# Performance work log

Hardware: AMD Instinct MI355X
Metric: run time of the kernel (lower is better)

Reference implementation:

```python
import jax, jax.numpy as jnp
import numpy as np

B, N, D = 256, 50, 128
N_NODE, MAX_ATTR = 50000, 2000
ALPHA = 0.2  # LeakyReLU negative slope
STDV = 1.0 / np.sqrt(D)  # reset_parameters uniform(-stdv, stdv)
NEG = -9e15


def setup_inputs() -> dict:
    key = jax.random.key(0)
    ks = jax.random.split(key, 10)
    uni = lambda k, shp: jax.random.uniform(k, shp, jnp.float32, -STDV, STDV)
    return {
        "inputs": jax.random.randint(ks[0], (B, N), 0, N_NODE),
        "adj": jax.random.randint(ks[1], (B, N, N), 0, 5),
        "mask_item": jax.random.randint(ks[2], (B, N), 0, 2),
        "A_attr_sess": jax.random.normal(ks[3], (B, MAX_ATTR), jnp.float32),
        "embedding": uni(ks[4], (N_NODE, D)),
        "attr_embedding": uni(ks[5], (MAX_ATTR, D)),
        "a0": uni(ks[6], (D,)),
        "a1": uni(ks[7], (D,)),
        "a2": uni(ks[8], (D,)),
        "a3": uni(ks[9], (D,)),
    }


def reference(inputs, adj, mask_item, A_attr_sess, embedding, attr_embedding, a0, a1, a2, a3):
    h = embedding[inputs]  # [B, N, D]
    # (h.repeat(1,1,N) * h.repeat(1,N,1)).view(B,N,N,D) == outer elementwise product h_i * h_j
    a_in = jax.nn.leaky_relu(h[:, :, None, :] * h[:, None, :, :], ALPHA)  # [B,N,N,D]
    a_all = jnp.stack([a0, a1, a2, a3], axis=-1)  # [D, 4]
    e = jnp.einsum('bijd,dk->bijk', a_in, a_all)  # [B,N,N,4]
    alpha = jnp.full(adj.shape, NEG, dtype=e.dtype)
    alpha = jnp.where(adj == 1, e[..., 0], alpha)
    alpha = jnp.where(adj == 2, e[..., 1], alpha)
    alpha = jnp.where(adj == 3, e[..., 2], alpha)
    alpha = jnp.where(adj == 4, e[..., 3], alpha)
    alpha = jax.nn.softmax(alpha, axis=-1)
    output = jnp.einsum('bij,bjd->bid', alpha, h)  # [B, N, D]
    attr_sess = A_attr_sess @ attr_embedding  # [B, D]
    return output, attr_sess
```

## Files before the change

### kernel.cpp

```cpp
#include <hip/hip_runtime.h>
#include <math.h>

#define BB 256
#define NN 50
#define DD 128
#define MAXA 2000
#define NEGV -9e15f
#define NATTR 256

#define H_S   136
#define HT_S  72
#define AL_S  72

#define H_OFF   0
#define HT_OFF  (64 * H_S)
#define AL_OFF  (HT_OFF + 128 * HT_S)
#define ADJ_OFF (AL_OFF + 64 * AL_S)
#define LDS_US  (ADJ_OFF + 64 * 64)

typedef __attribute__((ext_vector_type(8))) short        s8b;
typedef __attribute__((ext_vector_type(4))) float        f32x4;
typedef __attribute__((ext_vector_type(4))) unsigned int u32x4;

static __device__ __forceinline__ unsigned short f2bf(float x) {
    unsigned int u = __float_as_uint(x);
    u = u + 0x7fffu + ((u >> 16) & 1u);
    return (unsigned short)(u >> 16);
}
static __device__ __forceinline__ float bf2f(unsigned int s) {
    return __uint_as_float(s << 16);
}
static __device__ __forceinline__ unsigned int pack2(float lo, float hi) {
    return (unsigned)f2bf(lo) | ((unsigned)f2bf(hi) << 16);
}
static __device__ __forceinline__ f32x4 mfma16(u32x4 a, u32x4 b, f32x4 c) {
    return __builtin_amdgcn_mfma_f32_16x16x32_bf16(
        __builtin_bit_cast(s8b, a), __builtin_bit_cast(s8b, b), c, 0, 0, 0);
}

__global__ __launch_bounds__(256) void sg_fused_kernel(
    const int* __restrict__ inputs,
    const int* __restrict__ adj,
    const float* __restrict__ A_attr,
    const float* __restrict__ embedding,
    const float* __restrict__ attr_emb,
    const float* __restrict__ a0,
    const float* __restrict__ a1,
    const float* __restrict__ a2,
    const float* __restrict__ a3,
    float* __restrict__ out,
    float* __restrict__ ws)
{
    __shared__ __align__(16) unsigned short sh[LDS_US];
    const int blk  = blockIdx.x;
    const int tid  = threadIdx.x;
    const int w    = tid >> 6;
    const int lane = tid & 63;
    const int g    = lane >> 4;
    const int c    = lane & 15;
    const int goff = g * 8;

    if (blk >= NATTR) {
        const int b = blk - NATTR;

        const int  i_   = lane;
        const bool live = (i_ < NN);
        int node = 0;
        if (live) node = inputs[b * NN + i_];
        float4 gv[8];
        #pragma unroll
        for (int n = 0; n < 8; ++n) {
            gv[n] = make_float4(0.f, 0.f, 0.f, 0.f);
            if (live) gv[n] = *(const float4*)(embedding + (size_t)node * DD + (w * 8 + n) * 4);
        }
        for (int idx = tid; idx < 4096; idx += 256) {
            const int i = idx >> 6, j = idx & 63;
            int a = 0;
            if (i < NN && j < NN) a = adj[(size_t)b * (NN * NN) + i * NN + j];
            sh[ADJ_OFF + idx] = (unsigned short)a;
        }
        #pragma unroll
        for (int n = 0; n < 8; ++n) {
            const int d4 = w * 8 + n;
            const unsigned short b0 = f2bf(gv[n].x), b1 = f2bf(gv[n].y);
            const unsigned short b2 = f2bf(gv[n].z), b3 = f2bf(gv[n].w);
            *(uint2*)(sh + H_OFF + i_ * H_S + d4 * 4) =
                make_uint2((unsigned)b0 | ((unsigned)b1 << 16),
                           (unsigned)b2 | ((unsigned)b3 << 16));
            sh[HT_OFF + (d4 * 4 + 0) * HT_S + i_] = b0;
            sh[HT_OFF + (d4 * 4 + 1) * HT_S + i_] = b1;
            sh[HT_OFF + (d4 * 4 + 2) * HT_S + i_] = b2;
            sh[HT_OFF + (d4 * 4 + 3) * HT_S + i_] = b3;
        }
        __syncthreads();

        u32x4 hA[4];
        float hf[4][8], hb[4][8];
        #pragma unroll
        for (int dt = 0; dt < 4; ++dt) {
            hA[dt] = *(const u32x4*)(const void*)(sh + H_OFF + (w * 16 + c) * H_S + dt * 32 + goff);
            #pragma unroll
            for (int p = 0; p < 4; ++p) {
                const unsigned int hp = hA[dt][p];
                hf[dt][2 * p]     = bf2f(hp & 0xffffu);
                hf[dt][2 * p + 1] = bf2f(hp >> 16);
                hb[dt][2 * p]     = fabsf(hf[dt][2 * p]);
                hb[dt][2 * p + 1] = fabsf(hf[dt][2 * p + 1]);
            }
        }
        f32x4 accS[4][4];
        #pragma unroll
        for (int jt = 0; jt < 4; ++jt)
            #pragma unroll
            for (int k = 0; k < 4; ++k) accS[jt][k] = (f32x4){0.f, 0.f, 0.f, 0.f};

        #pragma unroll
        for (int pass = 0; pass < 2; ++pass) {
            u32x4 Uf[4][2], Vf[4][2];
            #pragma unroll
            for (int kk = 0; kk < 2; ++kk) {
                const int k = pass * 2 + kk;
                const float* ap = (k == 0) ? a0 : (k == 1) ? a1 : (k == 2) ? a2 : a3;
                #pragma unroll
                for (int dt = 0; dt < 4; ++dt) {
                    const float4 aL = *(const float4*)(ap + dt * 32 + goff);
                    const float4 aH = *(const float4*)(ap + dt * 32 + goff + 4);
                    const float a8[8] = {aL.x, aL.y, aL.z, aL.w, aH.x, aH.y, aH.z, aH.w};
                    u32x4 U, V;
                    #pragma unroll
                    for (int p = 0; p < 4; ++p) {
                        U[p] = pack2(0.6f * a8[2 * p] * hf[dt][2 * p],
                                     0.6f * a8[2 * p + 1] * hf[dt][2 * p + 1]);
                        V[p] = pack2(0.4f * a8[2 * p] * hb[dt][2 * p],
                                     0.4f * a8[2 * p + 1] * hb[dt][2 * p + 1]);
                    }
                    Uf[dt][kk] = U; Vf[dt][kk] = V;
                }
            }
            #pragma unroll
            for (int jt = 0; jt < 4; ++jt) {
                #pragma unroll
                for (int dt = 0; dt < 4; ++dt) {
                    const u32x4 hB = *(const u32x4*)(const void*)(sh + H_OFF + (jt * 16 + c) * H_S + dt * 32 + goff);
                    u32x4 hBa;
                    #pragma unroll
                    for (int p = 0; p < 4; ++p) hBa[p] = hB[p] & 0x7fff7fffu;
                    accS[jt][pass * 2 + 0] = mfma16(Uf[dt][0], hB,  accS[jt][pass * 2 + 0]);
                    accS[jt][pass * 2 + 0] = mfma16(Vf[dt][0], hBa, accS[jt][pass * 2 + 0]);
                    accS[jt][pass * 2 + 1] = mfma16(Uf[dt][1], hB,  accS[jt][pass * 2 + 1]);
                    accS[jt][pass * 2 + 1] = mfma16(Vf[dt][1], hBa, accS[jt][pass * 2 + 1]);
                }
            }
        }

        float s_[4][4];
        #pragma unroll
        for (int jt = 0; jt < 4; ++jt) {
            #pragma unroll
            for (int reg = 0; reg < 4; ++reg) {
                const int il = w * 16 + g * 4 + reg;
                const int j  = jt * 16 + c;
                const int a  = (int)sh[ADJ_OFF + il * 64 + j];
                float sv = (a == 1) ? accS[jt][0][reg] : (a == 2) ? accS[jt][1][reg]
                         : (a == 3) ? accS[jt][2][reg] : (a == 4) ? accS[jt][3][reg] : NEGV;
                if (j >= NN) sv = -INFINITY;
                s_[jt][reg] = sv;
            }
        }
        #pragma unroll
        for (int reg = 0; reg < 4; ++reg) {
            float m = fmaxf(fmaxf(s_[0][reg], s_[1][reg]), fmaxf(s_[2][reg], s_[3][reg]));
            m = fmaxf(m, __shfl_xor(m, 1));
            m = fmaxf(m, __shfl_xor(m, 2));
            m = fmaxf(m, __shfl_xor(m, 4));
            m = fmaxf(m, __shfl_xor(m, 8));
            const float p0 = __expf(s_[0][reg] - m);
            const float p1 = __expf(s_[1][reg] - m);
            const float p2 = __expf(s_[2][reg] - m);
            const float p3 = __expf(s_[3][reg] - m);
            float sum = (p0 + p1) + (p2 + p3);
            sum += __shfl_xor(sum, 1);
            sum += __shfl_xor(sum, 2);
            sum += __shfl_xor(sum, 4);
            sum += __shfl_xor(sum, 8);
            const float r  = 1.0f / sum;
            const int  il  = w * 16 + g * 4 + reg;
            sh[AL_OFF + il * AL_S +  0 + c] = f2bf(p0 * r);
            sh[AL_OFF + il * AL_S + 16 + c] = f2bf(p1 * r);
            sh[AL_OFF + il * AL_S + 32 + c] = f2bf(p2 * r);
            sh[AL_OFF + il * AL_S + 48 + c] = f2bf(p3 * r);
        }

        const int il = w * 16 + c;
        const u32x4 pa0 = *(const u32x4*)(const void*)(sh + AL_OFF + il * AL_S + goff);
        const u32x4 pa1 = *(const u32x4*)(const void*)(sh + AL_OFF + il * AL_S + 32 + goff);
        #pragma unroll
        for (int nt = 0; nt < 8; ++nt) {
            const u32x4 v0 = *(const u32x4*)(const void*)(sh + HT_OFF + (nt * 16 + c) * HT_S + goff);
            const u32x4 v1 = *(const u32x4*)(const void*)(sh + HT_OFF + (nt * 16 + c) * HT_S + 32 + goff);
            f32x4 accp = (f32x4){0.f, 0.f, 0.f, 0.f};
            accp = mfma16(pa0, v0, accp);
            accp = mfma16(pa1, v1, accp);
            #pragma unroll
            for (int reg = 0; reg < 4; ++reg) {
                const int ig = w * 16 + g * 4 + reg;
                if (ig < NN)
                    out[((size_t)b * NN + ig) * DD + nt * 16 + c] = accp[reg];
            }
        }
    } else {
        const int mg = blk >> 4;
        const int ks = blk & 15;
        const int m0 = mg * 16;
        const int wd = w * 32;
        const float* Arow = A_attr + (size_t)(m0 + c) * MAXA;

        f32x4 acc2[2];
        acc2[0] = (f32x4){0.f, 0.f, 0.f, 0.f};
        acc2[1] = (f32x4){0.f, 0.f, 0.f, 0.f};

        #pragma unroll
        for (int q = 0; q < 4; ++q) {
            const int s = ks + q * 16;
            if (s >= 63) break;
            const int k0 = s * 32;
            const float4 aL = *(const float4*)(Arow + k0 + goff);
            const float4 aH = *(const float4*)(Arow + k0 + goff + 4);
            u32x4 af;
            af[0] = pack2(aL.x, aL.y); af[1] = pack2(aL.z, aL.w);
            af[2] = pack2(aH.x, aH.y); af[3] = pack2(aH.z, aH.w);
            #pragma unroll
            for (int ntl = 0; ntl < 2; ++ntl) {
                const int col = wd + ntl * 16 + c;
                float ev[8];
                #pragma unroll
                for (int p = 0; p < 8; ++p)
                    ev[p] = attr_emb[(size_t)(k0 + goff + p) * DD + col];
                u32x4 bf_;
                bf_[0] = pack2(ev[0], ev[1]); bf_[1] = pack2(ev[2], ev[3]);
                bf_[2] = pack2(ev[4], ev[5]); bf_[3] = pack2(ev[6], ev[7]);
                acc2[ntl] = mfma16(af, bf_, acc2[ntl]);
            }
        }
        float* pt = ws + (size_t)blk * (16 * DD);
        #pragma unroll
        for (int ntl = 0; ntl < 2; ++ntl)
            #pragma unroll
            for (int reg = 0; reg < 4; ++reg)
                pt[(g * 4 + reg) * DD + wd + ntl * 16 + c] = acc2[ntl][reg];
    }
}

__global__ __launch_bounds__(256) void attr_reduce_kernel(
    const float* __restrict__ ws, float* __restrict__ attr_out)
{
    const int idx = blockIdx.x * 256 + threadIdx.x;
    const int m  = idx >> 7;
    const int d  = idx & 127;
    const int mg = m >> 4;
    const int r  = m & 15;
    const size_t base = (size_t)mg * 16 * (16 * DD) + r * DD + d;
    float v = 0.f;
    #pragma unroll
    for (int ks = 0; ks < 16; ++ks)
        v += ws[base + (size_t)ks * (16 * DD)];
    attr_out[(size_t)m * DD + d] = v;
}

extern "C" void kernel_launch(void* const* d_in, const int* in_sizes, int n_in,
                              void* d_out, int out_size, void* d_ws, size_t ws_size,
                              hipStream_t stream) {
    const int*   inputs    = (const int*)  d_in[0];
    const int*   adj       = (const int*)  d_in[1];
    const float* A_attr    = (const float*)d_in[3];
    const float* embedding = (const float*)d_in[4];
    const float* attr_emb  = (const float*)d_in[5];
    const float* a0        = (const float*)d_in[6];
    const float* a1        = (const float*)d_in[7];
    const float* a2        = (const float*)d_in[8];
    const float* a3        = (const float*)d_in[9];

    float* out      = (float*)d_out;
    float* attr_out = out + (size_t)BB * NN * DD;
    float* ws       = (float*)d_ws;

    sg_fused_kernel<<<NATTR + BB, 256, 0, stream>>>(inputs, adj, A_attr, embedding,
                                                    attr_emb, a0, a1, a2, a3,
                                                    out, ws);
    attr_reduce_kernel<<<128, 256, 0, stream>>>(ws, attr_out);
}
```

Baseline: 22.36 us.

## Use hardware bf16 pack conversion, schedule graph blocks first, guard attr tail

Replaces the software round-to-nearest bf16 conversion with the packed hardware convert instruction, which cuts ALU work in staging and softmax. Reorders the grid so the heavier per-session attention blocks are dispatched before the attr GEMM blocks, to improve the load-balance tail. Restructures the attr k-loop into three unguarded chunks plus a bounds-guarded final chunk. The guard avoids out-of-range reads past the attribute dimension. The hardware conversion's rounding behaviour may differ slightly from the old software rounding.

```diff
diff --git a/kernel.cpp b/kernel.cpp
--- a/kernel.cpp
+++ b/kernel.cpp
@@ -22,16 +22,13 @@
 typedef __attribute__((ext_vector_type(4))) float        f32x4;
 typedef __attribute__((ext_vector_type(4))) unsigned int u32x4;
 
-static __device__ __forceinline__ unsigned short f2bf(float x) {
-    unsigned int u = __float_as_uint(x);
-    u = u + 0x7fffu + ((u >> 16) & 1u);
-    return (unsigned short)(u >> 16);
+static __device__ __forceinline__ unsigned int pack2(float lo, float hi) {
+    unsigned int r;
+    asm("v_cvt_pk_bf16_f32 %0, %1, %2" : "=v"(r) : "v"(lo), "v"(hi));
+    return r;
 }
 static __device__ __forceinline__ float bf2f(unsigned int s) {
     return __uint_as_float(s << 16);
-}
-static __device__ __forceinline__ unsigned int pack2(float lo, float hi) {
-    return (unsigned)f2bf(lo) | ((unsigned)f2bf(hi) << 16);
 }
 static __device__ __forceinline__ f32x4 mfma16(u32x4 a, u32x4 b, f32x4 c) {
     return __builtin_amdgcn_mfma_f32_16x16x32_bf16(
@@ -60,8 +57,8 @@
     const int c    = lane & 15;
     const int goff = g * 8;
 
-    if (blk >= NATTR) {
-        const int b = blk - NATTR;
+    if (blk < BB) {
+        const int b = blk;
 
         const int  i_   = lane;
         const bool live = (i_ < NN);
@@ -82,15 +79,13 @@
         #pragma unroll
         for (int n = 0; n < 8; ++n) {
             const int d4 = w * 8 + n;
-            const unsigned short b0 = f2bf(gv[n].x), b1 = f2bf(gv[n].y);
-            const unsigned short b2 = f2bf(gv[n].z), b3 = f2bf(gv[n].w);
-            *(uint2*)(sh + H_OFF + i_ * H_S + d4 * 4) =
-                make_uint2((unsigned)b0 | ((unsigned)b1 << 16),
-                           (unsigned)b2 | ((unsigned)b3 << 16));
-            sh[HT_OFF + (d4 * 4 + 0) * HT_S + i_] = b0;
-            sh[HT_OFF + (d4 * 4 + 1) * HT_S + i_] = b1;
-            sh[HT_OFF + (d4 * 4 + 2) * HT_S + i_] = b2;
-            sh[HT_OFF + (d4 * 4 + 3) * HT_S + i_] = b3;
+            const unsigned int pk01 = pack2(gv[n].x, gv[n].y);
+            const unsigned int pk23 = pack2(gv[n].z, gv[n].w);
+            *(uint2*)(sh + H_OFF + i_ * H_S + d4 * 4) = make_uint2(pk01, pk23);
+            sh[HT_OFF + (d4 * 4 + 0) * HT_S + i_] = (unsigned short)pk01;
+            sh[HT_OFF + (d4 * 4 + 1) * HT_S + i_] = (unsigned short)(pk01 >> 16);
+            sh[HT_OFF + (d4 * 4 + 2) * HT_S + i_] = (unsigned short)pk23;
+            sh[HT_OFF + (d4 * 4 + 3) * HT_S + i_] = (unsigned short)(pk23 >> 16);
         }
         __syncthreads();
 
@@ -185,10 +180,10 @@
             sum += __shfl_xor(sum, 8);
             const float r  = 1.0f / sum;
             const int  il  = w * 16 + g * 4 + reg;
-            sh[AL_OFF + il * AL_S +  0 + c] = f2bf(p0 * r);
-            sh[AL_OFF + il * AL_S + 16 + c] = f2bf(p1 * r);
-            sh[AL_OFF + il * AL_S + 32 + c] = f2bf(p2 * r);
-            sh[AL_OFF + il * AL_S + 48 + c] = f2bf(p3 * r);
+            sh[AL_OFF + il * AL_S +  0 + c] = (unsigned short)pack2(p0 * r, p0 * r);
+            sh[AL_OFF + il * AL_S + 16 + c] = (unsigned short)pack2(p1 * r, p1 * r);
+            sh[AL_OFF + il * AL_S + 32 + c] = (unsigned short)pack2(p2 * r, p2 * r);
+            sh[AL_OFF + il * AL_S + 48 + c] = (unsigned short)pack2(p3 * r, p3 * r);
         }
 
         const int il = w * 16 + c;
@@ -209,8 +204,9 @@
             }
         }
     } else {
-        const int mg = blk >> 4;
-        const int ks = blk & 15;
+        const int ablk = blk - BB;
+        const int mg = ablk >> 4;
+        const int ks = ablk & 15;
         const int m0 = mg * 16;
         const int wd = w * 32;
         const float* Arow = A_attr + (size_t)(m0 + c) * MAXA;
@@ -219,13 +215,11 @@
         acc2[0] = (f32x4){0.f, 0.f, 0.f, 0.f};
         acc2[1] = (f32x4){0.f, 0.f, 0.f, 0.f};
 
-        #pragma unroll
-        for (int q = 0; q < 4; ++q) {
-            const int s = ks + q * 16;
-            if (s >= 63) break;
-            const int k0 = s * 32;
-            const float4 aL = *(const float4*)(Arow + k0 + goff);
-            const float4 aH = *(const float4*)(Arow + k0 + goff + 4);
+        auto do_chunk = [&](int k0, bool guard) {
+            float4 aL = make_float4(0.f, 0.f, 0.f, 0.f);
+            float4 aH = make_float4(0.f, 0.f, 0.f, 0.f);
+            if (!guard || k0 + goff + 3 < MAXA) aL = *(const float4*)(Arow + k0 + goff);
+            if (!guard || k0 + goff + 7 < MAXA) aH = *(const float4*)(Arow + k0 + goff + 4);
             u32x4 af;
             af[0] = pack2(aL.x, aL.y); af[1] = pack2(aL.z, aL.w);
             af[2] = pack2(aH.x, aH.y); af[3] = pack2(aH.z, aH.w);
@@ -234,15 +228,21 @@
                 const int col = wd + ntl * 16 + c;
                 float ev[8];
                 #pragma unroll
-                for (int p = 0; p < 8; ++p)
-                    ev[p] = attr_emb[(size_t)(k0 + goff + p) * DD + col];
+                for (int p = 0; p < 8; ++p) {
+                    const int kr = k0 + goff + p;
+                    ev[p] = (!guard || kr < MAXA) ? attr_emb[(size_t)kr * DD + col] : 0.f;
+                }
                 u32x4 bf_;
                 bf_[0] = pack2(ev[0], ev[1]); bf_[1] = pack2(ev[2], ev[3]);
                 bf_[2] = pack2(ev[4], ev[5]); bf_[3] = pack2(ev[6], ev[7]);
                 acc2[ntl] = mfma16(af, bf_, acc2[ntl]);
             }
-        }
-        float* pt = ws + (size_t)blk * (16 * DD);
+        };
+        #pragma unroll
+        for (int q = 0; q < 3; ++q) do_chunk((ks + q * 16) * 32, false);
+        if (ks + 48 < 63) do_chunk((ks + 48) * 32, (ks + 48) == 62);
+
+        float* pt = ws + (size_t)ablk * (16 * DD);
         #pragma unroll
         for (int ntl = 0; ntl < 2; ++ntl)
             #pragma unroll
@@ -284,7 +284,7 @@
     float* attr_out = out + (size_t)BB * NN * DD;
     float* ws       = (float*)d_ws;
 
-    sg_fused_kernel<<<NATTR + BB, 256, 0, stream>>>(inputs, adj, A_attr, embedding,
+    sg_fused_kernel<<<BB + NATTR, 256, 0, stream>>>(inputs, adj, A_attr, embedding,
                                                     attr_emb, a0, a1, a2, a3,
                                                     out, ws);
     attr_reduce_kernel<<<128, 256, 0, stream>>>(ws, attr_out);
```

Measured after the change: 21.73 us. -2.8%, faster.
